# Optimization experiments

Hardware: AMD Instinct MI355X
Metric: run time of the kernel (lower is better)

Reference implementation:

```python
import jax, jax.numpy as jnp
import numpy as np

N_NODES = 50000
N_EDGES = 800000
NFEAT, NHID1, NHID2, NHID3, NCLASS = 128, 128, 128, 64, 32


def _glorot(key, fan_in, fan_out):
    lim = 1.0 / np.sqrt(fan_in)
    return jax.random.uniform(key, (fan_in, fan_out), jnp.float32, -lim, lim)


def setup_inputs() -> dict:
    key = jax.random.key(0)
    ks = jax.random.split(key, 12)
    x = jax.random.normal(ks[0], (N_NODES, NFEAT), jnp.float32)
    edge_src = jax.random.randint(ks[1], (N_EDGES,), 0, N_NODES, jnp.int32)
    edge_dst = jax.random.randint(ks[2], (N_EDGES,), 0, N_NODES, jnp.int32)
    edge_val = jax.random.uniform(ks[3], (N_EDGES,), jnp.float32)
    W1 = _glorot(ks[4], NFEAT, NHID1)
    W2 = _glorot(ks[5], NHID1, NHID2)
    W3 = _glorot(ks[6], NHID2, NHID3)
    W4 = _glorot(ks[7], NHID3, NCLASS)
    b1 = jnp.zeros((NHID1,), jnp.float32)
    b2 = jnp.zeros((NHID2,), jnp.float32)
    b3 = jnp.zeros((NHID3,), jnp.float32)
    b4 = jnp.zeros((NCLASS,), jnp.float32)
    return {"x": x, "edge_src": edge_src, "edge_dst": edge_dst, "edge_val": edge_val,
            "W1": W1, "b1": b1, "W2": W2, "b2": b2, "W3": W3, "b3": b3, "W4": W4, "b4": b4}


def _gc_layer(h, W, b, src, dst, val):
    # support = h @ W ; out = adj @ support + b  (adj in COO form)
    support = h @ W                                   # [N, d_out]
    msgs = support[src] * val[:, None]                # [E, d_out] irregular gather
    agg = jax.ops.segment_sum(msgs, dst, num_segments=N_NODES)  # scatter-add
    return agg + b


def reference(x, edge_src, edge_dst, edge_val, W1, b1, W2, b2, W3, b3, W4, b4):
    h = jax.nn.relu(_gc_layer(x, W1, b1, edge_src, edge_dst, edge_val))
    h = jax.nn.relu(_gc_layer(h, W2, b2, edge_src, edge_dst, edge_val))
    h = jax.nn.relu(_gc_layer(h, W3, b3, edge_src, edge_dst, edge_val))
    h = _gc_layer(h, W4, b4, edge_src, edge_dst, edge_val)
    return h
```

## Files before the change

### kernel.cpp

```cpp
#include <hip/hip_runtime.h>

constexpr int NNODES = 50000;
constexpr int NEDGES = 800000;
constexpr int CAP = 64;

constexpr int NPART = 8;
constexpr int PSIZE = NNODES / NPART;
constexpr int FCH = 1024;
constexpr int QCAP = 320;

constexpr int FILL_ITEMS = ((NEDGES + FCH - 1) / FCH) * NPART;
constexpr int TILE_ITEMS = (NNODES + 63) / 64;
constexpr int PREP_TOT = NNODES + 43008;

typedef __attribute__((ext_vector_type(8))) short short8;
typedef __attribute__((ext_vector_type(8))) unsigned short ushort8;
typedef __attribute__((ext_vector_type(4))) float f32x4;

__device__ __forceinline__ unsigned short f2b(float f) {
    unsigned int u = __float_as_uint(f);
    u += 0x7FFFu + ((u >> 16) & 1u);
    return (unsigned short)(u >> 16);
}
__device__ __forceinline__ float b2f(unsigned short u) {
    return __uint_as_float(((unsigned int)u) << 16);
}

template <int N, int K>
__device__ __forceinline__ void pack_one(int idx, const float* __restrict__ W,
                                         unsigned short* __restrict__ Wp) {
    constexpr int KS = K / 32;
    int j = idx & 7;
    int lane = (idx >> 3) & 63;
    int t = idx >> 9;
    int nt = t / KS, ks = t % KS;
    int n = nt * 16 + (lane & 15);
    int k = ks * 32 + (lane >> 4) * 8 + j;
    Wp[idx] = f2b(W[(size_t)k * N + n]);
}

__global__ __launch_bounds__(256) void prep_kernel(int* __restrict__ cursor,
        const float* __restrict__ W1, const float* __restrict__ W2,
        const float* __restrict__ W3, const float* __restrict__ W4,
        unsigned short* __restrict__ Wp1, unsigned short* __restrict__ Wp2,
        unsigned short* __restrict__ Wp3, unsigned short* __restrict__ Wp4) {
    int idx = blockIdx.x * 256 + threadIdx.x;
    if (idx < NNODES) { cursor[idx] = 0; return; }
    int p = idx - NNODES;
    if (p < 16384) pack_one<128, 128>(p, W1, Wp1);
    else if (p < 32768) pack_one<128, 128>(p - 16384, W2, Wp2);
    else if (p < 40960) pack_one<64, 128>(p - 32768, W3, Wp3);
    else if (p < 43008 && p >= 40960) pack_one<32, 64>(p - 40960, W4, Wp4);
}

template <int N, int K, bool AF32>
__device__ __forceinline__ void gemm_item(int t, const void* __restrict__ Hv,
                                          const unsigned short* __restrict__ Wp,
                                          unsigned short* __restrict__ Sb) {
    constexpr int NT = N / 16, KS = K / 32;
    const int lane = threadIdx.x & 63;
    const int wave = threadIdx.x >> 6;
    const int waveRow = t * 64 + wave * 16;
    const int m = lane & 15, quad = lane >> 4;
    int arow = waveRow + m;
    if (arow >= NNODES) arow = NNODES - 1;

    f32x4 acc[NT];
#pragma unroll
    for (int nt = 0; nt < NT; ++nt) acc[nt] = (f32x4){0.f, 0.f, 0.f, 0.f};

#pragma unroll
    for (int ks = 0; ks < KS; ++ks) {
        short8 a;
        if (AF32) {
            const float* hp = (const float*)Hv + (size_t)arow * K + ks * 32 + quad * 8;
            float4 a0 = *reinterpret_cast<const float4*>(hp);
            float4 a1 = *reinterpret_cast<const float4*>(hp + 4);
            a[0] = (short)f2b(a0.x); a[1] = (short)f2b(a0.y);
            a[2] = (short)f2b(a0.z); a[3] = (short)f2b(a0.w);
            a[4] = (short)f2b(a1.x); a[5] = (short)f2b(a1.y);
            a[6] = (short)f2b(a1.z); a[7] = (short)f2b(a1.w);
        } else {
            a = *reinterpret_cast<const short8*>(
                (const unsigned short*)Hv + (size_t)arow * K + ks * 32 + quad * 8);
        }
#pragma unroll
        for (int nt = 0; nt < NT; ++nt) {
            short8 b = *reinterpret_cast<const short8*>(Wp + ((nt * KS + ks) * 64 + lane) * 8);
            acc[nt] = __builtin_amdgcn_mfma_f32_16x16x32_bf16(a, b, acc[nt], 0, 0, 0);
        }
    }

#pragma unroll
    for (int reg = 0; reg < 4; ++reg) {
        int grow = waveRow + quad * 4 + reg;
        if (grow < NNODES) {
#pragma unroll
            for (int nt = 0; nt < NT; ++nt)
                Sb[(size_t)grow * N + nt * 16 + m] = f2b(acc[nt][reg]);
        }
    }
}

__global__ __launch_bounds__(256) void fill_gemm1_kernel(
        const int* __restrict__ src, const int* __restrict__ dst,
        const float* __restrict__ val, int* __restrict__ cursor,
        int2* __restrict__ buckets,
        const float* __restrict__ x, const unsigned short* __restrict__ Wp1,
        unsigned short* __restrict__ Q) {
    __shared__ int q_e[QCAP];
    __shared__ int q_d[QCAP];
    __shared__ int qcount;

    if (blockIdx.x >= FILL_ITEMS) {
        gemm_item<128, 128, true>(blockIdx.x - FILL_ITEMS, x, Wp1, Q);
        return;
    }

    if (threadIdx.x == 0) qcount = 0;
    __syncthreads();

    int part = blockIdx.x % NPART;
    int chunk = blockIdx.x / NPART;
    int lo = part * PSIZE, hi = lo + PSIZE;
    int e0 = chunk * FCH + threadIdx.x * 4;

    int4 d4 = make_int4(-1, -1, -1, -1);
    if (e0 + 3 < NEDGES) {
        d4 = *reinterpret_cast<const int4*>(dst + e0);
    } else if (e0 < NEDGES) {
        d4.x = dst[e0];
        if (e0 + 1 < NEDGES) d4.y = dst[e0 + 1];
        if (e0 + 2 < NEDGES) d4.z = dst[e0 + 2];
    }
    int dd[4] = {d4.x, d4.y, d4.z, d4.w};
#pragma unroll
    for (int i = 0; i < 4; ++i) {
        int d = dd[i];
        if (d >= lo && d < hi) {
            int pos = atomicAdd(&qcount, 1);
            if (pos < QCAP) {
                q_e[pos] = e0 + i;
                q_d[pos] = d;
            } else {
                int e = e0 + i;
                int p = atomicAdd(&cursor[d], 1);
                if (p < CAP)
                    buckets[(size_t)d * CAP + p] = make_int2(src[e], __float_as_int(val[e]));
            }
        }
    }
    __syncthreads();

    int n = qcount < QCAP ? qcount : QCAP;
    for (int i = threadIdx.x; i < n; i += 256) {
        int e = q_e[i];
        int d = q_d[i];
        int s = src[e];
        float v = val[e];
        int p = atomicAdd(&cursor[d], 1);
        if (p < CAP)
            buckets[(size_t)d * CAP + p] = make_int2(s, __float_as_int(v));
    }
}

template <int NIN, int NOUT>
__global__ __launch_bounds__(256) void agg_gemm_kernel(
        const unsigned short* __restrict__ Sprev, const int2* __restrict__ buckets,
        const int* __restrict__ counts, const float* __restrict__ bias,
        const unsigned short* __restrict__ Wp, unsigned short* __restrict__ Snext) {
    constexpr int NCH = NIN / 8;
    constexpr int R = 256 / NCH;
    constexpr int LROW = NIN + 8;
    constexpr int KS = NIN / 32;
    constexpr int NT = NOUT / 16;
    constexpr int RT = R / 16;
    constexpr int TILES = RT * NT;
    __shared__ unsigned short htile[R * LROW];

    const int nodeBase = blockIdx.x * R;

    {
        int nl = threadIdx.x / NCH;
        int cg = threadIdx.x % NCH;
        int node = nodeBase + nl;
        float acc[8];
        if (node < NNODES) {
#pragma unroll
            for (int t = 0; t < 8; ++t) acc[t] = bias[cg * 8 + t];
            int cnt = counts[node];
            if (cnt > CAP) cnt = CAP;
            const int2* eb = buckets + (size_t)node * CAP;
            int j = 0;
            for (; j + 4 <= cnt; j += 4) {
                int4 ea = *reinterpret_cast<const int4*>(eb + j);
                int4 ec = *reinterpret_cast<const int4*>(eb + j + 2);
                const ushort8 m0 = *reinterpret_cast<const ushort8*>(Sprev + (size_t)ea.x * NIN + cg * 8);
                const ushort8 m1 = *reinterpret_cast<const ushort8*>(Sprev + (size_t)ea.z * NIN + cg * 8);
                const ushort8 m2 = *reinterpret_cast<const ushort8*>(Sprev + (size_t)ec.x * NIN + cg * 8);
                const ushort8 m3 = *reinterpret_cast<const ushort8*>(Sprev + (size_t)ec.z * NIN + cg * 8);
                float v0 = __int_as_float(ea.y), v1 = __int_as_float(ea.w);
                float v2 = __int_as_float(ec.y), v3 = __int_as_float(ec.w);
#pragma unroll
                for (int t = 0; t < 8; ++t) {
                    acc[t] = fmaf(b2f(m0[t]), v0, acc[t]);
                    acc[t] = fmaf(b2f(m1[t]), v1, acc[t]);
                    acc[t] = fmaf(b2f(m2[t]), v2, acc[t]);
                    acc[t] = fmaf(b2f(m3[t]), v3, acc[t]);
                }
            }
            for (; j < cnt; ++j) {
                int2 e = eb[j];
                float v = __int_as_float(e.y);
                const ushort8 mr = *reinterpret_cast<const ushort8*>(Sprev + (size_t)e.x * NIN + cg * 8);
#pragma unroll
                for (int t = 0; t < 8; ++t) acc[t] = fmaf(b2f(mr[t]), v, acc[t]);
            }
        } else {
#pragma unroll
            for (int t = 0; t < 8; ++t) acc[t] = 0.f;
        }
        ushort8 o;
#pragma unroll
        for (int t = 0; t < 8; ++t) o[t] = f2b(fmaxf(acc[t], 0.f));
        *reinterpret_cast<ushort8*>(&htile[nl * LROW + cg * 8]) = o;
    }
    __syncthreads();

    {
        const int lane = threadIdx.x & 63, wave = threadIdx.x >> 6;
        const int m = lane & 15, quad = lane >> 4;
        for (int t = wave; t < TILES; t += 4) {
            int rt = t / NT, nt = t % NT;
            f32x4 acc = (f32x4){0.f, 0.f, 0.f, 0.f};
#pragma unroll
            for (int ks = 0; ks < KS; ++ks) {
                short8 a = *reinterpret_cast<const short8*>(
                    &htile[(rt * 16 + m) * LROW + ks * 32 + quad * 8]);
                short8 b = *reinterpret_cast<const short8*>(Wp + ((nt * KS + ks) * 64 + lane) * 8);
                acc = __builtin_amdgcn_mfma_f32_16x16x32_bf16(a, b, acc, 0, 0, 0);
            }
#pragma unroll
            for (int reg = 0; reg < 4; ++reg) {
                int grow = nodeBase + rt * 16 + quad * 4 + reg;
                if (grow < NNODES)
                    Snext[(size_t)grow * NOUT + nt * 16 + m] = f2b(acc[reg]);
            }
        }
    }
}

__global__ __launch_bounds__(256) void agg_out_kernel(const unsigned short* __restrict__ Sb,
        const int2* __restrict__ buckets, const int* __restrict__ counts,
        const float* __restrict__ bias, float* __restrict__ outp) {
    constexpr int N = 32;
    int node = blockIdx.x * 64 + threadIdx.x / 4;
    int cg = threadIdx.x % 4;
    if (node >= NNODES) return;
    int cnt = counts[node];
    if (cnt > CAP) cnt = CAP;
    const int2* eb = buckets + (size_t)node * CAP;
    float acc[8];
#pragma unroll
    for (int t = 0; t < 8; ++t) acc[t] = bias[cg * 8 + t];

    int j = 0;
    for (; j + 4 <= cnt; j += 4) {
        int4 ea = *reinterpret_cast<const int4*>(eb + j);
        int4 ec = *reinterpret_cast<const int4*>(eb + j + 2);
        const ushort8 m0 = *reinterpret_cast<const ushort8*>(Sb + (size_t)ea.x * N + cg * 8);
        const ushort8 m1 = *reinterpret_cast<const ushort8*>(Sb + (size_t)ea.z * N + cg * 8);
        const ushort8 m2 = *reinterpret_cast<const ushort8*>(Sb + (size_t)ec.x * N + cg * 8);
        const ushort8 m3 = *reinterpret_cast<const ushort8*>(Sb + (size_t)ec.z * N + cg * 8);
        float v0 = __int_as_float(ea.y), v1 = __int_as_float(ea.w);
        float v2 = __int_as_float(ec.y), v3 = __int_as_float(ec.w);
#pragma unroll
        for (int t = 0; t < 8; ++t) {
            acc[t] = fmaf(b2f(m0[t]), v0, acc[t]);
            acc[t] = fmaf(b2f(m1[t]), v1, acc[t]);
            acc[t] = fmaf(b2f(m2[t]), v2, acc[t]);
            acc[t] = fmaf(b2f(m3[t]), v3, acc[t]);
        }
    }
    for (; j < cnt; ++j) {
        int2 e = eb[j];
        float v = __int_as_float(e.y);
        const ushort8 mr = *reinterpret_cast<const ushort8*>(Sb + (size_t)e.x * N + cg * 8);
#pragma unroll
        for (int t = 0; t < 8; ++t) acc[t] = fmaf(b2f(mr[t]), v, acc[t]);
    }

    float* op = outp + (size_t)node * N + cg * 8;
    *reinterpret_cast<float4*>(op) = make_float4(acc[0], acc[1], acc[2], acc[3]);
    *reinterpret_cast<float4*>(op + 4) = make_float4(acc[4], acc[5], acc[6], acc[7]);
}

extern "C" void kernel_launch(void* const* d_in, const int* in_sizes, int n_in,
                              void* d_out, int out_size, void* d_ws, size_t ws_size,
                              hipStream_t stream) {
    const float* x   = (const float*)d_in[0];
    const int*   src = (const int*)d_in[1];
    const int*   dst = (const int*)d_in[2];
    const float* val = (const float*)d_in[3];
    const float* W1  = (const float*)d_in[4];
    const float* b1  = (const float*)d_in[5];
    const float* W2  = (const float*)d_in[6];
    const float* b2  = (const float*)d_in[7];
    const float* W3  = (const float*)d_in[8];
    const float* b3  = (const float*)d_in[9];
    const float* W4  = (const float*)d_in[10];
    const float* b4  = (const float*)d_in[11];
    float* out = (float*)d_out;

    unsigned short* P = (unsigned short*)d_ws;
    unsigned short* Q = P + (size_t)NNODES * 128;
    int2* buckets = (int2*)(Q + (size_t)NNODES * 128);
    unsigned short* Wp1 = (unsigned short*)(buckets + (size_t)NNODES * CAP);
    unsigned short* Wp2 = Wp1 + 128 * 128;
    unsigned short* Wp3 = Wp2 + 128 * 128;
    unsigned short* Wp4 = Wp3 + 128 * 64;
    int* cursor = (int*)(Wp4 + 64 * 32);

    const dim3 blk(256);

    prep_kernel<<<(PREP_TOT + 255) / 256, blk, 0, stream>>>(cursor, W1, W2, W3, W4,
                                                            Wp1, Wp2, Wp3, Wp4);
    fill_gemm1_kernel<<<FILL_ITEMS + TILE_ITEMS, blk, 0, stream>>>(
        src, dst, val, cursor, buckets, x, Wp1, Q);
    agg_gemm_kernel<128, 128><<<(NNODES + 15) / 16, blk, 0, stream>>>(
        Q, buckets, cursor, b1, Wp2, P);
    agg_gemm_kernel<128, 64><<<(NNODES + 15) / 16, blk, 0, stream>>>(
        P, buckets, cursor, b2, Wp3, Q);
    agg_gemm_kernel<64, 32><<<(NNODES + 31) / 32, blk, 0, stream>>>(
        Q, buckets, cursor, b3, Wp4, P);
    agg_out_kernel<<<(NNODES + 63) / 64, blk, 0, stream>>>(P, buckets, cursor, b4, out);
}
```

Measured before the change: 227.2 us.

## Pack edge records into 32 bits and interleave GEMM tiles with fill blocks

Each bucketed edge is now stored in one 32-bit word: a 16-bit source index plus the edge weight rounded to bf16. This halves bucket storage and the bucket reads in all four aggregation kernels. The fill blocks load src and val as vectors up front instead of doing per-edge gathers later. GEMM tiles are interleaved with fill chunks in the grid, and the cursor reset moves to hipMemsetAsync. The cost is lower precision on edge weights and a hard requirement that the node count fit in 16 bits.

```diff
diff --git a/kernel.cpp b/kernel.cpp
--- a/kernel.cpp
+++ b/kernel.cpp
@@ -9,9 +9,9 @@
 constexpr int FCH = 1024;
 constexpr int QCAP = 320;
 
-constexpr int FILL_ITEMS = ((NEDGES + FCH - 1) / FCH) * NPART;
+constexpr int CHUNKS = (NEDGES + FCH - 1) / FCH;
 constexpr int TILE_ITEMS = (NNODES + 63) / 64;
-constexpr int PREP_TOT = NNODES + 43008;
+constexpr int PACK_TOT = 43008;
 
 typedef __attribute__((ext_vector_type(8))) short short8;
 typedef __attribute__((ext_vector_type(8))) unsigned short ushort8;
@@ -24,6 +24,9 @@
 }
 __device__ __forceinline__ float b2f(unsigned short u) {
     return __uint_as_float(((unsigned int)u) << 16);
+}
+__device__ __forceinline__ float recval(unsigned int rec) {
+    return __uint_as_float(rec & 0xFFFF0000u);
 }
 
 template <int N, int K>
@@ -39,18 +42,16 @@
     Wp[idx] = f2b(W[(size_t)k * N + n]);
 }
 
-__global__ __launch_bounds__(256) void prep_kernel(int* __restrict__ cursor,
+__global__ __launch_bounds__(256) void prep_kernel(
         const float* __restrict__ W1, const float* __restrict__ W2,
         const float* __restrict__ W3, const float* __restrict__ W4,
         unsigned short* __restrict__ Wp1, unsigned short* __restrict__ Wp2,
         unsigned short* __restrict__ Wp3, unsigned short* __restrict__ Wp4) {
-    int idx = blockIdx.x * 256 + threadIdx.x;
-    if (idx < NNODES) { cursor[idx] = 0; return; }
-    int p = idx - NNODES;
+    int p = blockIdx.x * 256 + threadIdx.x;
     if (p < 16384) pack_one<128, 128>(p, W1, Wp1);
     else if (p < 32768) pack_one<128, 128>(p - 16384, W2, Wp2);
     else if (p < 40960) pack_one<64, 128>(p - 32768, W3, Wp3);
-    else if (p < 43008 && p >= 40960) pack_one<32, 64>(p - 40960, W4, Wp4);
+    else if (p < 43008) pack_one<32, 64>(p - 40960, W4, Wp4);
 }
 
 template <int N, int K, bool AF32>
@@ -105,48 +106,54 @@
 __global__ __launch_bounds__(256) void fill_gemm1_kernel(
         const int* __restrict__ src, const int* __restrict__ dst,
         const float* __restrict__ val, int* __restrict__ cursor,
-        int2* __restrict__ buckets,
+        unsigned int* __restrict__ buckets,
         const float* __restrict__ x, const unsigned short* __restrict__ Wp1,
         unsigned short* __restrict__ Q) {
-    __shared__ int q_e[QCAP];
+    __shared__ unsigned int q_rec[QCAP];
     __shared__ int q_d[QCAP];
     __shared__ int qcount;
 
-    if (blockIdx.x >= FILL_ITEMS) {
-        gemm_item<128, 128, true>(blockIdx.x - FILL_ITEMS, x, Wp1, Q);
+    const int g = blockIdx.x / 9;
+    const int r = blockIdx.x % 9;
+    if (r == 0) {
+        gemm_item<128, 128, true>(g, x, Wp1, Q);
         return;
     }
 
     if (threadIdx.x == 0) qcount = 0;
     __syncthreads();
 
-    int part = blockIdx.x % NPART;
-    int chunk = blockIdx.x / NPART;
-    int lo = part * PSIZE, hi = lo + PSIZE;
-    int e0 = chunk * FCH + threadIdx.x * 4;
+    const int part = blockIdx.x & 7;
+    const int lo = part * PSIZE, hi = lo + PSIZE;
+    const int e0 = g * FCH + threadIdx.x * 4;
 
     int4 d4 = make_int4(-1, -1, -1, -1);
+    int4 s4 = make_int4(0, 0, 0, 0);
+    float4 v4 = make_float4(0.f, 0.f, 0.f, 0.f);
     if (e0 + 3 < NEDGES) {
         d4 = *reinterpret_cast<const int4*>(dst + e0);
+        s4 = *reinterpret_cast<const int4*>(src + e0);
+        v4 = *reinterpret_cast<const float4*>(val + e0);
     } else if (e0 < NEDGES) {
-        d4.x = dst[e0];
-        if (e0 + 1 < NEDGES) d4.y = dst[e0 + 1];
-        if (e0 + 2 < NEDGES) d4.z = dst[e0 + 2];
+        d4.x = dst[e0]; s4.x = src[e0]; v4.x = val[e0];
+        if (e0 + 1 < NEDGES) { d4.y = dst[e0 + 1]; s4.y = src[e0 + 1]; v4.y = val[e0 + 1]; }
+        if (e0 + 2 < NEDGES) { d4.z = dst[e0 + 2]; s4.z = src[e0 + 2]; v4.z = val[e0 + 2]; }
     }
     int dd[4] = {d4.x, d4.y, d4.z, d4.w};
+    int ss[4] = {s4.x, s4.y, s4.z, s4.w};
+    float vv[4] = {v4.x, v4.y, v4.z, v4.w};
 #pragma unroll
     for (int i = 0; i < 4; ++i) {
         int d = dd[i];
         if (d >= lo && d < hi) {
+            unsigned int rec = (unsigned int)ss[i] | ((unsigned int)f2b(vv[i]) << 16);
             int pos = atomicAdd(&qcount, 1);
             if (pos < QCAP) {
-                q_e[pos] = e0 + i;
+                q_rec[pos] = rec;
                 q_d[pos] = d;
             } else {
-                int e = e0 + i;
                 int p = atomicAdd(&cursor[d], 1);
-                if (p < CAP)
-                    buckets[(size_t)d * CAP + p] = make_int2(src[e], __float_as_int(val[e]));
+                if (p < CAP) buckets[(size_t)d * CAP + p] = rec;
             }
         }
     }
@@ -154,19 +161,16 @@
 
     int n = qcount < QCAP ? qcount : QCAP;
     for (int i = threadIdx.x; i < n; i += 256) {
-        int e = q_e[i];
         int d = q_d[i];
-        int s = src[e];
-        float v = val[e];
+        unsigned int rec = q_rec[i];
         int p = atomicAdd(&cursor[d], 1);
-        if (p < CAP)
-            buckets[(size_t)d * CAP + p] = make_int2(s, __float_as_int(v));
+        if (p < CAP) buckets[(size_t)d * CAP + p] = rec;
     }
 }
 
 template <int NIN, int NOUT>
 __global__ __launch_bounds__(256) void agg_gemm_kernel(
-        const unsigned short* __restrict__ Sprev, const int2* __restrict__ buckets,
+        const unsigned short* __restrict__ Sprev, const unsigned int* __restrict__ buckets,
         const int* __restrict__ counts, const float* __restrict__ bias,
         const unsigned short* __restrict__ Wp, unsigned short* __restrict__ Snext) {
     constexpr int NCH = NIN / 8;
@@ -190,17 +194,16 @@
             for (int t = 0; t < 8; ++t) acc[t] = bias[cg * 8 + t];
             int cnt = counts[node];
             if (cnt > CAP) cnt = CAP;
-            const int2* eb = buckets + (size_t)node * CAP;
+            const unsigned int* eb = buckets + (size_t)node * CAP;
             int j = 0;
             for (; j + 4 <= cnt; j += 4) {
-                int4 ea = *reinterpret_cast<const int4*>(eb + j);
-                int4 ec = *reinterpret_cast<const int4*>(eb + j + 2);
-                const ushort8 m0 = *reinterpret_cast<const ushort8*>(Sprev + (size_t)ea.x * NIN + cg * 8);
-                const ushort8 m1 = *reinterpret_cast<const ushort8*>(Sprev + (size_t)ea.z * NIN + cg * 8);
-                const ushort8 m2 = *reinterpret_cast<const ushort8*>(Sprev + (size_t)ec.x * NIN + cg * 8);
-                const ushort8 m3 = *reinterpret_cast<const ushort8*>(Sprev + (size_t)ec.z * NIN + cg * 8);
-                float v0 = __int_as_float(ea.y), v1 = __int_as_float(ea.w);
-                float v2 = __int_as_float(ec.y), v3 = __int_as_float(ec.w);
+                uint4 ea = *reinterpret_cast<const uint4*>(eb + j);
+                const ushort8 m0 = *reinterpret_cast<const ushort8*>(Sprev + (size_t)(ea.x & 0xFFFF) * NIN + cg * 8);
+                const ushort8 m1 = *reinterpret_cast<const ushort8*>(Sprev + (size_t)(ea.y & 0xFFFF) * NIN + cg * 8);
+                const ushort8 m2 = *reinterpret_cast<const ushort8*>(Sprev + (size_t)(ea.z & 0xFFFF) * NIN + cg * 8);
+                const ushort8 m3 = *reinterpret_cast<const ushort8*>(Sprev + (size_t)(ea.w & 0xFFFF) * NIN + cg * 8);
+                float v0 = recval(ea.x), v1 = recval(ea.y);
+                float v2 = recval(ea.z), v3 = recval(ea.w);
 #pragma unroll
                 for (int t = 0; t < 8; ++t) {
                     acc[t] = fmaf(b2f(m0[t]), v0, acc[t]);
@@ -210,9 +213,9 @@
                 }
             }
             for (; j < cnt; ++j) {
-                int2 e = eb[j];
-                float v = __int_as_float(e.y);
-                const ushort8 mr = *reinterpret_cast<const ushort8*>(Sprev + (size_t)e.x * NIN + cg * 8);
+                unsigned int rec = eb[j];
+                float v = recval(rec);
+                const ushort8 mr = *reinterpret_cast<const ushort8*>(Sprev + (size_t)(rec & 0xFFFF) * NIN + cg * 8);
 #pragma unroll
                 for (int t = 0; t < 8; ++t) acc[t] = fmaf(b2f(mr[t]), v, acc[t]);
             }
@@ -251,7 +254,7 @@
 }
 
 __global__ __launch_bounds__(256) void agg_out_kernel(const unsigned short* __restrict__ Sb,
-        const int2* __restrict__ buckets, const int* __restrict__ counts,
+        const unsigned int* __restrict__ buckets, const int* __restrict__ counts,
         const float* __restrict__ bias, float* __restrict__ outp) {
     constexpr int N = 32;
     int node = blockIdx.x * 64 + threadIdx.x / 4;
@@ -259,21 +262,20 @@
     if (node >= NNODES) return;
     int cnt = counts[node];
     if (cnt > CAP) cnt = CAP;
-    const int2* eb = buckets + (size_t)node * CAP;
+    const unsigned int* eb = buckets + (size_t)node * CAP;
     float acc[8];
 #pragma unroll
     for (int t = 0; t < 8; ++t) acc[t] = bias[cg * 8 + t];
 
     int j = 0;
     for (; j + 4 <= cnt; j += 4) {
-        int4 ea = *reinterpret_cast<const int4*>(eb + j);
-        int4 ec = *reinterpret_cast<const int4*>(eb + j + 2);
-        const ushort8 m0 = *reinterpret_cast<const ushort8*>(Sb + (size_t)ea.x * N + cg * 8);
-        const ushort8 m1 = *reinterpret_cast<const ushort8*>(Sb + (size_t)ea.z * N + cg * 8);
-        const ushort8 m2 = *reinterpret_cast<const ushort8*>(Sb + (size_t)ec.x * N + cg * 8);
-        const ushort8 m3 = *reinterpret_cast<const ushort8*>(Sb + (size_t)ec.z * N + cg * 8);
-        float v0 = __int_as_float(ea.y), v1 = __int_as_float(ea.w);
-        float v2 = __int_as_float(ec.y), v3 = __int_as_float(ec.w);
+        uint4 ea = *reinterpret_cast<const uint4*>(eb + j);
+        const ushort8 m0 = *reinterpret_cast<const ushort8*>(Sb + (size_t)(ea.x & 0xFFFF) * N + cg * 8);
+        const ushort8 m1 = *reinterpret_cast<const ushort8*>(Sb + (size_t)(ea.y & 0xFFFF) * N + cg * 8);
+        const ushort8 m2 = *reinterpret_cast<const ushort8*>(Sb + (size_t)(ea.z & 0xFFFF) * N + cg * 8);
+        const ushort8 m3 = *reinterpret_cast<const ushort8*>(Sb + (size_t)(ea.w & 0xFFFF) * N + cg * 8);
+        float v0 = recval(ea.x), v1 = recval(ea.y);
+        float v2 = recval(ea.z), v3 = recval(ea.w);
 #pragma unroll
         for (int t = 0; t < 8; ++t) {
             acc[t] = fmaf(b2f(m0[t]), v0, acc[t]);
@@ -283,9 +285,9 @@
         }
     }
     for (; j < cnt; ++j) {
-        int2 e = eb[j];
-        float v = __int_as_float(e.y);
-        const ushort8 mr = *reinterpret_cast<const ushort8*>(Sb + (size_t)e.x * N + cg * 8);
+        unsigned int rec = eb[j];
+        float v = recval(rec);
+        const ushort8 mr = *reinterpret_cast<const ushort8*>(Sb + (size_t)(rec & 0xFFFF) * N + cg * 8);
 #pragma unroll
         for (int t = 0; t < 8; ++t) acc[t] = fmaf(b2f(mr[t]), v, acc[t]);
     }
@@ -314,7 +316,7 @@
 
     unsigned short* P = (unsigned short*)d_ws;
     unsigned short* Q = P + (size_t)NNODES * 128;
-    int2* buckets = (int2*)(Q + (size_t)NNODES * 128);
+    unsigned int* buckets = (unsigned int*)(Q + (size_t)NNODES * 128);
     unsigned short* Wp1 = (unsigned short*)(buckets + (size_t)NNODES * CAP);
     unsigned short* Wp2 = Wp1 + 128 * 128;
     unsigned short* Wp3 = Wp2 + 128 * 128;
@@ -323,9 +325,10 @@
 
     const dim3 blk(256);
 
-    prep_kernel<<<(PREP_TOT + 255) / 256, blk, 0, stream>>>(cursor, W1, W2, W3, W4,
+    hipMemsetAsync(cursor, 0, NNODES * sizeof(int), stream);
+    prep_kernel<<<(PACK_TOT + 255) / 256, blk, 0, stream>>>(W1, W2, W3, W4,
                                                             Wp1, Wp2, Wp3, Wp4);
-    fill_gemm1_kernel<<<FILL_ITEMS + TILE_ITEMS, blk, 0, stream>>>(
+    fill_gemm1_kernel<<<CHUNKS * 9, blk, 0, stream>>>(
         src, dst, val, cursor, buckets, x, Wp1, Q);
     agg_gemm_kernel<128, 128><<<(NNODES + 15) / 16, blk, 0, stream>>>(
         Q, buckets, cursor, b1, Wp2, P);
```

After: 221.1 us. -2.6%, faster.
